# Kernel tuning notes

Measured on AMD Instinct MI355X. Metric: run time of the kernel, lower is better.

Reference implementation:

```python
import jax, jax.numpy as jnp
import numpy as np

N = 16384          # total nodes (128 graphs x 128 ops)
G = 128            # number of graphs
NPG = N // G       # nodes per graph
DIN = 64           # op_input_dim
H = 64             # hidden_dim
BN_EPS = 1e-5


def setup_inputs() -> dict:
    key = jax.random.key(0)
    ks = jax.random.split(key, 16)
    x = jax.random.normal(ks[0], (N, DIN), dtype=jnp.float32)
    # sparse-ish 0/1 adjacency stored dense (as torch.mm path expects); add self-loops so degrees > 0
    u = jax.random.uniform(ks[1], (N, N), dtype=jnp.float32)
    adj = jnp.maximum((u < 0.004).astype(jnp.float32), jnp.eye(N, dtype=jnp.float32))
    # graph_pool: [G, N] average-pooling matrix (block rows of 1/NPG)
    rows = jnp.repeat(jnp.arange(G), NPG)
    graph_pool = jnp.zeros((G, N), jnp.float32).at[rows, jnp.arange(N)].set(1.0 / NPG)
    s = 0.05
    params = {}
    dims_in = [DIN, H]
    for l in range(2):
        d_in = dims_in[l]
        params[f"W1_{l}"] = jax.random.normal(ks[2 + 6 * l], (d_in, H), jnp.float32) * s
        params[f"b1_{l}"] = jnp.zeros((H,), jnp.float32)
        params[f"g1_{l}"] = jnp.ones((H,), jnp.float32)
        params[f"be1_{l}"] = jnp.zeros((H,), jnp.float32)
        params[f"W2_{l}"] = jax.random.normal(ks[3 + 6 * l], (H, H), jnp.float32) * s
        params[f"b2_{l}"] = jnp.zeros((H,), jnp.float32)
        params[f"g_{l}"] = jnp.ones((H,), jnp.float32)   # outer BN gamma
        params[f"be_{l}"] = jnp.zeros((H,), jnp.float32)  # outer BN beta
    return {"x": x, "adj": adj, "graph_pool": graph_pool, **params}


def _bn(h, g, b):
    # training-mode BatchNorm1d over node axis (biased var), eps=1e-5
    m = jnp.mean(h, axis=0)
    v = jnp.var(h, axis=0)
    return g * (h - m) * jax.lax.rsqrt(v + BN_EPS) + b


def _mlp(h, W1, b1, g1, be1, W2, b2):
    # 2-layer MLP: Linear -> BN -> ReLU -> Linear
    return jax.nn.relu(_bn(h @ W1 + b1, g1, be1)) @ W2 + b2


def reference(x, adj, graph_pool,
              W1_0, b1_0, g1_0, be1_0, W2_0, b2_0, g_0, be_0,
              W1_1, b1_1, g1_1, be1_1, W2_1, b2_1, g_1, be_1):
    deg = adj @ jnp.ones((adj.shape[0], 1), adj.dtype)  # [N,1]
    h = x
    layers = [
        (W1_0, b1_0, g1_0, be1_0, W2_0, b2_0, g_0, be_0),
        (W1_1, b1_1, g1_1, be1_1, W2_1, b2_1, g_1, be_1),
    ]
    for (W1, b1, g1, be1, W2, b2, g, be) in layers:
        pooled = (adj @ h) / deg                 # average neighbor aggregation
        pooled_rep = _mlp(pooled, W1, b1, g1, be1, W2, b2)
        h = jax.nn.relu(_bn(pooled_rep, g, be))
    h_nodes = h
    pooled_h = graph_pool @ h                    # [G, H] graph readout
    return (pooled_h, h_nodes)
```

## Files before the change

### kernel.cpp

```cpp
#include <hip/hip_runtime.h>
#include <hip/hip_bf16.h>
#include <stdint.h>

#define N_NODES 16384
#define GG      128
#define HD      64
#define MAXD    192
#define BN_EPS  1e-5f

typedef unsigned short u16;
typedef unsigned int   u32;
typedef unsigned long long u64;

__device__ __forceinline__ float bf2f(u16 u) {
    union { u32 i; float f; } c; c.i = ((u32)u) << 16; return c.f;
}
__device__ __forceinline__ float ldp(const void* p, int i, int flag) {
    return flag ? ((const float*)p)[i] : bf2f(((const u16*)p)[i]);
}

__global__ void k_init(const u32* __restrict__ adj32, double* __restrict__ statsD,
                       int* __restrict__ flag) {
    int i = threadIdx.x;
    if (i < 512) statsD[i] = 0.0;
    if (i == 0) *flag = ((adj32[0] & 0xFFFFu) == 0) ? 1 : 0;
}

__global__ __launch_bounds__(256) void k_agg(
    const void* __restrict__ adjv, const void* __restrict__ xv,
    float* __restrict__ pooled, u16* __restrict__ cols,
    int* __restrict__ cnt, float* __restrict__ invdeg,
    const int* __restrict__ flagp)
{
    const int wave = threadIdx.x >> 6;
    const int lane = threadIdx.x & 63;
    const int row  = blockIdx.x * 4 + wave;
    u16* __restrict__ crow = cols + (size_t)row * MAXD;
    const int flag = *flagp;

    float acc = 0.f;
    int count = 0;

    if (flag) {
        const u32* __restrict__ arow = (const u32*)adjv + (size_t)row * N_NODES;
        const float* __restrict__ x = (const float*)xv;
        uint4 nxt = *(const uint4*)(arow + lane * 4);
        for (int c = 0; c < N_NODES; c += 256) {
            uint4 raw = nxt;
            if (c + 256 < N_NODES)
                nxt = *(const uint4*)(arow + c + 256 + lane * 4);
            const u32 w[4] = {raw.x, raw.y, raw.z, raw.w};
            #pragma unroll
            for (int e = 0; e < 4; ++e) {
                u64 mask = __ballot(w[e] != 0);
                while (mask) {
                    int b = __builtin_ctzll(mask);
                    mask &= mask - 1;
                    int j = c + b * 4 + e;
                    acc += x[(size_t)j * HD + lane];
                    if (lane == 0 && count < MAXD) crow[count] = (u16)j;
                    ++count;
                }
            }
        }
    } else {
        const u16* __restrict__ arow = (const u16*)adjv + (size_t)row * N_NODES;
        const u16* __restrict__ x = (const u16*)xv;
        uint4 nxt = *(const uint4*)(arow + lane * 8);
        for (int c = 0; c < N_NODES; c += 512) {
            uint4 raw = nxt;
            if (c + 512 < N_NODES)
                nxt = *(const uint4*)(arow + c + 512 + lane * 8);
            const u32 w[4] = {raw.x, raw.y, raw.z, raw.w};
            #pragma unroll
            for (int e = 0; e < 8; ++e) {
                u16 u = (u16)(w[e >> 1] >> ((e & 1) * 16));
                u64 mask = __ballot(u != 0);
                while (mask) {
                    int b = __builtin_ctzll(mask);
                    mask &= mask - 1;
                    int j = c + b * 8 + e;
                    acc += bf2f(x[(size_t)j * HD + lane]);
                    if (lane == 0 && count < MAXD) crow[count] = (u16)j;
                    ++count;
                }
            }
        }
    }
    float inv = 1.f / (float)count;
    pooled[(size_t)row * HD + lane] = acc * inv;
    if (lane == 0) { cnt[row] = (count < MAXD) ? count : MAXD; invdeg[row] = inv; }
}

__global__ __launch_bounds__(256) void k_mm(
    const float* __restrict__ src, const void* __restrict__ W,
    const void* __restrict__ bias, float* __restrict__ dst,
    const int* __restrict__ flagp)
{
    __shared__ float Wf[64 * 64];
    __shared__ float S[4 * 64];
    const int tid = threadIdx.x;
    const int flag = *flagp;
    for (int i = tid; i < 64 * 64; i += 256) Wf[i] = ldp(W, i, flag);
    const int rbase = blockIdx.x * 4;
    S[tid] = src[(size_t)rbase * 64 + tid];
    __syncthreads();
    const int f = tid & 63, r = tid >> 6;
    float acc = ldp(bias, f, flag);
    #pragma unroll
    for (int k = 0; k < 64; ++k)
        acc = fmaf(S[r * 64 + k], Wf[k * 64 + f], acc);
    dst[(size_t)(rbase + r) * 64 + f] = acc;
}

__global__ __launch_bounds__(256) void k_stats(
    const float* __restrict__ src, double* __restrict__ statsOut)
{
    __shared__ double shs[256];
    __shared__ double shq[256];
    const int tid = threadIdx.x;
    const int f = tid & 63, rsub = tid >> 6;
    const int rbase = blockIdx.x * 64;
    double s = 0.0, q = 0.0;
    for (int r = rsub; r < 64; r += 4) {
        float v = src[(size_t)(rbase + r) * 64 + f];
        s += (double)v;
        q += (double)v * (double)v;
    }
    shs[tid] = s; shq[tid] = q;
    __syncthreads();
    if (tid < 64) {
        double S = shs[tid] + shs[64 + tid] + shs[128 + tid] + shs[192 + tid];
        double Q = shq[tid] + shq[64 + tid] + shq[128 + tid] + shq[192 + tid];
        atomicAdd(&statsOut[tid], S);
        atomicAdd(&statsOut[64 + tid], Q);
    }
}

__global__ __launch_bounds__(256) void k_bnrelu(
    const float* __restrict__ src, const double* __restrict__ stats,
    const void* __restrict__ g, const void* __restrict__ be,
    float* __restrict__ dst, const int* __restrict__ flagp)
{
    __shared__ float ac[128];
    const int tid = threadIdx.x;
    const int flag = *flagp;
    if (tid < 64) {
        double m = stats[tid] * (1.0 / N_NODES);
        double v = stats[64 + tid] * (1.0 / N_NODES) - m * m;
        float A = ldp(g, tid, flag) / sqrtf((float)v + BN_EPS);
        ac[tid] = A;
        ac[64 + tid] = ldp(be, tid, flag) - (float)m * A;
    }
    __syncthreads();
    const size_t idx = ((size_t)blockIdx.x * 256 + tid) * 4;
    const int f0 = (int)(idx & 63);
    float4 t = *(const float4*)&src[idx];
    const float4 A4 = *(const float4*)&ac[f0];
    const float4 C4 = *(const float4*)&ac[64 + f0];
    float4 r;
    r.x = fmaxf(fmaf(A4.x, t.x, C4.x), 0.f);
    r.y = fmaxf(fmaf(A4.y, t.y, C4.y), 0.f);
    r.z = fmaxf(fmaf(A4.z, t.z, C4.z), 0.f);
    r.w = fmaxf(fmaf(A4.w, t.w, C4.w), 0.f);
    *(float4*)&dst[idx] = r;
}

__global__ __launch_bounds__(256) void k_spmm(
    const float* __restrict__ h, const u16* __restrict__ cols,
    const int* __restrict__ cnt, const float* __restrict__ invdeg,
    float* __restrict__ pooled)
{
    const int wave = threadIdx.x >> 6, lane = threadIdx.x & 63;
    const int row = blockIdx.x * 4 + wave;
    const u16* __restrict__ crow = cols + (size_t)row * MAXD;
    const int n = cnt[row];
    float acc = 0.f;
    for (int k = 0; k < n; ++k)
        acc += h[(size_t)crow[k] * HD + lane];
    pooled[(size_t)row * HD + lane] = acc * invdeg[row];
}

__global__ __launch_bounds__(1024) void k_pool(
    const void* __restrict__ gpv, const float* __restrict__ h,
    float* __restrict__ out, const int* __restrict__ flagp)
{
    __shared__ float red[16 * 64];
    const int g = blockIdx.x;
    const int wave = threadIdx.x >> 6, lane = threadIdx.x & 63;
    const int flag = *flagp;
    float acc = 0.f;
    const int jb0 = wave * (N_NODES / 16);
    if (flag) {
        const float* __restrict__ grow = (const float*)gpv + (size_t)g * N_NODES;
        for (int jb = jb0; jb < jb0 + N_NODES / 16; jb += 4) {
            float4 raw = *(const float4*)(grow + jb);
            if (raw.x != 0.f) acc += raw.x * h[(size_t)(jb + 0) * HD + lane];
            if (raw.y != 0.f) acc += raw.y * h[(size_t)(jb + 1) * HD + lane];
            if (raw.z != 0.f) acc += raw.z * h[(size_t)(jb + 2) * HD + lane];
            if (raw.w != 0.f) acc += raw.w * h[(size_t)(jb + 3) * HD + lane];
        }
    } else {
        const u16* __restrict__ grow = (const u16*)gpv + (size_t)g * N_NODES;
        for (int jb = jb0; jb < jb0 + N_NODES / 16; jb += 8) {
            uint4 raw = *(const uint4*)(grow + jb);
            const u32 w[4] = {raw.x, raw.y, raw.z, raw.w};
            #pragma unroll
            for (int e = 0; e < 8; ++e) {
                u16 u = (u16)(w[e >> 1] >> ((e & 1) * 16));
                if (u) acc += bf2f(u) * h[(size_t)(jb + e) * HD + lane];
            }
        }
    }
    red[wave * 64 + lane] = acc;
    __syncthreads();
    if (wave == 0) {
        float s = 0.f;
        #pragma unroll
        for (int w2 = 0; w2 < 16; ++w2) s += red[w2 * 64 + lane];
        out[g * 64 + lane] = s;
    }
}

extern "C" void kernel_launch(void* const* d_in, const int* in_sizes, int n_in,
                              void* d_out, int out_size, void* d_ws, size_t ws_size,
                              hipStream_t stream)
{
    const void* x    = d_in[0];
    const void* adj  = d_in[1];
    const void* gp   = d_in[2];
    const void* W1_0 = d_in[3];
    const void* b1_0 = d_in[4];
    const void* g1_0 = d_in[5];
    const void* be1_0= d_in[6];
    const void* W2_0 = d_in[7];
    const void* b2_0 = d_in[8];
    const void* g_0  = d_in[9];
    const void* be_0 = d_in[10];
    const void* W1_1 = d_in[11];
    const void* b1_1 = d_in[12];
    const void* g1_1 = d_in[13];
    const void* be1_1= d_in[14];
    const void* W2_1 = d_in[15];
    const void* b2_1 = d_in[16];
    const void* g_1  = d_in[17];
    const void* be_1 = d_in[18];

    char* ws = (char*)d_ws;
    float*  P      = (float*) (ws);
    float*  A      = (float*) (ws + (4u  << 20));
    float*  B      = (float*) (ws + (8u  << 20));
    u16*    cols   = (u16*)   (ws + (12u << 20));
    int*    cnt    = (int*)   (ws + (18u << 20));
    float*  invdeg = (float*) (ws + (18u << 20) + 65536);
    double* sd     = (double*)(ws + (18u << 20) + 131072);
    int*    flag   = (int*)   (ws + (18u << 20) + 131072 + 4096);

    float* out_pool  = (float*)d_out;
    float* out_nodes = (float*)d_out + GG * HD;

    const int EB = (N_NODES * HD / 4) / 256;

    k_init<<<1, 512, 0, stream>>>((const u32*)adj, sd, flag);
    k_agg<<<N_NODES / 4, 256, 0, stream>>>(adj, x, P, cols, cnt, invdeg, flag);

    k_mm<<<N_NODES / 4, 256, 0, stream>>>(P, W1_0, b1_0, A, flag);
    k_stats<<<256, 256, 0, stream>>>(A, sd + 0);
    k_bnrelu<<<EB, 256, 0, stream>>>(A, sd + 0, g1_0, be1_0, B, flag);
    k_mm<<<N_NODES / 4, 256, 0, stream>>>(B, W2_0, b2_0, P, flag);
    k_stats<<<256, 256, 0, stream>>>(P, sd + 128);
    k_bnrelu<<<EB, 256, 0, stream>>>(P, sd + 128, g_0, be_0, A, flag);
    k_spmm<<<N_NODES / 4, 256, 0, stream>>>(A, cols, cnt, invdeg, B);
    k_mm<<<N_NODES / 4, 256, 0, stream>>>(B, W1_1, b1_1, P, flag);
    k_stats<<<256, 256, 0, stream>>>(P, sd + 256);
    k_bnrelu<<<EB, 256, 0, stream>>>(P, sd + 256, g1_1, be1_1, A, flag);
    k_mm<<<N_NODES / 4, 256, 0, stream>>>(A, W2_1, b2_1, B, flag);
    k_stats<<<256, 256, 0, stream>>>(B, sd + 384);
    k_bnrelu<<<EB, 256, 0, stream>>>(B, sd + 384, g_1, be_1, out_nodes, flag);
    k_pool<<<GG, 1024, 0, stream>>>(gp, out_nodes, out_pool, flag);
}
```

Measured before the change: 1.696 ms.

## Split adjacency aggregation into streaming scan with atomics and separate gather

Replaces the per-row wave scan, which interleaved ballot loops with dependent feature gathers, with a grid-stride kernel that streams the dense adjacency and appends nonzero column indices through per-row atomic counters. A separate gather kernel then sums neighbor features from the compacted lists, and the SpMM loops are unrolled by four. The aim is to turn the dominant 1 GiB adjacency read into a pure bandwidth-bound stream. In exchange it adds atomics, a nondeterministic neighbor order (so the float summation order varies), and an extra launch.

After: 1.778 ms. 4.8% more time.

```diff
diff --git a/kernel.cpp b/kernel.cpp
--- a/kernel.cpp
+++ b/kernel.cpp
@@ -19,77 +19,101 @@
     return flag ? ((const float*)p)[i] : bf2f(((const u16*)p)[i]);
 }
 
-__global__ void k_init(const u32* __restrict__ adj32, double* __restrict__ statsD,
-                       int* __restrict__ flag) {
-    int i = threadIdx.x;
-    if (i < 512) statsD[i] = 0.0;
-    if (i == 0) *flag = ((adj32[0] & 0xFFFFu) == 0) ? 1 : 0;
-}
-
-__global__ __launch_bounds__(256) void k_agg(
-    const void* __restrict__ adjv, const void* __restrict__ xv,
-    float* __restrict__ pooled, u16* __restrict__ cols,
-    int* __restrict__ cnt, float* __restrict__ invdeg,
-    const int* __restrict__ flagp)
-{
-    const int wave = threadIdx.x >> 6;
-    const int lane = threadIdx.x & 63;
-    const int row  = blockIdx.x * 4 + wave;
-    u16* __restrict__ crow = cols + (size_t)row * MAXD;
-    const int flag = *flagp;
-
-    float acc = 0.f;
-    int count = 0;
-
+__global__ __launch_bounds__(256) void k_init(
+    const u32* __restrict__ adj32, double* __restrict__ statsD,
+    int* __restrict__ cnt, int* __restrict__ flag)
+{
+    const int gid = blockIdx.x * 256 + threadIdx.x;
+    if (gid < N_NODES) cnt[gid] = 0;
+    if (gid < 512) statsD[gid] = 0.0;
+    if (gid == 0) *flag = ((adj32[0] & 0xFFFFu) == 0) ? 1 : 0;
+}
+
+__global__ __launch_bounds__(256) void k_scan(
+    const void* __restrict__ adjv, u16* __restrict__ cols,
+    int* __restrict__ cnt, const int* __restrict__ flagp)
+{
+    const int flag = *flagp;
+    const size_t stride = (size_t)gridDim.x * 256;
+    size_t i = (size_t)blockIdx.x * 256 + threadIdx.x;
     if (flag) {
-        const u32* __restrict__ arow = (const u32*)adjv + (size_t)row * N_NODES;
-        const float* __restrict__ x = (const float*)xv;
-        uint4 nxt = *(const uint4*)(arow + lane * 4);
-        for (int c = 0; c < N_NODES; c += 256) {
-            uint4 raw = nxt;
-            if (c + 256 < N_NODES)
-                nxt = *(const uint4*)(arow + c + 256 + lane * 4);
-            const u32 w[4] = {raw.x, raw.y, raw.z, raw.w};
-            #pragma unroll
-            for (int e = 0; e < 4; ++e) {
-                u64 mask = __ballot(w[e] != 0);
-                while (mask) {
-                    int b = __builtin_ctzll(mask);
-                    mask &= mask - 1;
-                    int j = c + b * 4 + e;
-                    acc += x[(size_t)j * HD + lane];
-                    if (lane == 0 && count < MAXD) crow[count] = (u16)j;
-                    ++count;
+        const uint4* __restrict__ a = (const uint4*)adjv;
+        const size_t total = (size_t)N_NODES * N_NODES / 4;
+        for (; i < total; i += stride) {
+            uint4 w = a[i];
+            if (w.x | w.y | w.z | w.w) {
+                size_t base = i * 4;
+                int row = (int)(base >> 14);
+                int col = (int)(base & 16383);
+                u16* crow = cols + (size_t)row * MAXD;
+                if (w.x) { int p = atomicAdd(&cnt[row], 1); if (p < MAXD) crow[p] = (u16)(col);     }
+                if (w.y) { int p = atomicAdd(&cnt[row], 1); if (p < MAXD) crow[p] = (u16)(col + 1); }
+                if (w.z) { int p = atomicAdd(&cnt[row], 1); if (p < MAXD) crow[p] = (u16)(col + 2); }
+                if (w.w) { int p = atomicAdd(&cnt[row], 1); if (p < MAXD) crow[p] = (u16)(col + 3); }
+            }
+        }
+    } else {
+        const uint4* __restrict__ a = (const uint4*)adjv;
+        const size_t total = (size_t)N_NODES * N_NODES / 8;
+        for (; i < total; i += stride) {
+            uint4 w = a[i];
+            if (w.x | w.y | w.z | w.w) {
+                size_t base = i * 8;
+                int row = (int)(base >> 14);
+                int col = (int)(base & 16383);
+                u16* crow = cols + (size_t)row * MAXD;
+                const u32 h[4] = {w.x, w.y, w.z, w.w};
+                #pragma unroll
+                for (int e = 0; e < 8; ++e) {
+                    if ((u16)(h[e >> 1] >> ((e & 1) * 16))) {
+                        int p = atomicAdd(&cnt[row], 1);
+                        if (p < MAXD) crow[p] = (u16)(col + e);
+                    }
                 }
             }
         }
+    }
+}
+
+__global__ __launch_bounds__(256) void k_gather(
+    const void* __restrict__ xv, const u16* __restrict__ cols,
+    int* __restrict__ cnt, float* __restrict__ invdeg,
+    float* __restrict__ pooled, const int* __restrict__ flagp)
+{
+    const int wave = threadIdx.x >> 6, lane = threadIdx.x & 63;
+    const int row = blockIdx.x * 4 + wave;
+    const int flag = *flagp;
+    const u16* __restrict__ crow = cols + (size_t)row * MAXD;
+    int n = cnt[row];
+    if (n > MAXD) n = MAXD;
+    float acc = 0.f;
+    int k = 0;
+    if (flag) {
+        const float* __restrict__ x = (const float*)xv;
+        for (; k + 4 <= n; k += 4) {
+            ushort4 j4 = *(const ushort4*)&crow[k];
+            float v0 = x[(size_t)j4.x * HD + lane];
+            float v1 = x[(size_t)j4.y * HD + lane];
+            float v2 = x[(size_t)j4.z * HD + lane];
+            float v3 = x[(size_t)j4.w * HD + lane];
+            acc += (v0 + v1) + (v2 + v3);
+        }
+        for (; k < n; ++k) acc += x[(size_t)crow[k] * HD + lane];
     } else {
-        const u16* __restrict__ arow = (const u16*)adjv + (size_t)row * N_NODES;
         const u16* __restrict__ x = (const u16*)xv;
-        uint4 nxt = *(const uint4*)(arow + lane * 8);
-        for (int c = 0; c < N_NODES; c += 512) {
-            uint4 raw = nxt;
-            if (c + 512 < N_NODES)
-                nxt = *(const uint4*)(arow + c + 512 + lane * 8);
-            const u32 w[4] = {raw.x, raw.y, raw.z, raw.w};
-            #pragma unroll
-            for (int e = 0; e < 8; ++e) {
-                u16 u = (u16)(w[e >> 1] >> ((e & 1) * 16));
-                u64 mask = __ballot(u != 0);
-                while (mask) {
-                    int b = __builtin_ctzll(mask);
-                    mask &= mask - 1;
-                    int j = c + b * 8 + e;
-                    acc += bf2f(x[(size_t)j * HD + lane]);
-                    if (lane == 0 && count < MAXD) crow[count] = (u16)j;
-                    ++count;
-                }
-            }
-        }
-    }
-    float inv = 1.f / (float)count;
+        for (; k + 4 <= n; k += 4) {
+            ushort4 j4 = *(const ushort4*)&crow[k];
+            float v0 = bf2f(x[(size_t)j4.x * HD + lane]);
+            float v1 = bf2f(x[(size_t)j4.y * HD + lane]);
+            float v2 = bf2f(x[(size_t)j4.z * HD + lane]);
+            float v3 = bf2f(x[(size_t)j4.w * HD + lane]);
+            acc += (v0 + v1) + (v2 + v3);
+        }
+        for (; k < n; ++k) acc += bf2f(x[(size_t)crow[k] * HD + lane]);
+    }
+    float inv = 1.f / (float)n;
     pooled[(size_t)row * HD + lane] = acc * inv;
-    if (lane == 0) { cnt[row] = (count < MAXD) ? count : MAXD; invdeg[row] = inv; }
+    if (lane == 0) { invdeg[row] = inv; if (cnt[row] > MAXD) cnt[row] = MAXD; }
 }
 
 __global__ __launch_bounds__(256) void k_mm(
@@ -176,8 +200,16 @@
     const u16* __restrict__ crow = cols + (size_t)row * MAXD;
     const int n = cnt[row];
     float acc = 0.f;
-    for (int k = 0; k < n; ++k)
-        acc += h[(size_t)crow[k] * HD + lane];
+    int k = 0;
+    for (; k + 4 <= n; k += 4) {
+        ushort4 j4 = *(const ushort4*)&crow[k];
+        float v0 = h[(size_t)j4.x * HD + lane];
+        float v1 = h[(size_t)j4.y * HD + lane];
+        float v2 = h[(size_t)j4.z * HD + lane];
+        float v3 = h[(size_t)j4.w * HD + lane];
+        acc += (v0 + v1) + (v2 + v3);
+    }
+    for (; k < n; ++k) acc += h[(size_t)crow[k] * HD + lane];
     pooled[(size_t)row * HD + lane] = acc * invdeg[row];
 }
 
@@ -261,8 +293,9 @@
 
     const int EB = (N_NODES * HD / 4) / 256;
 
-    k_init<<<1, 512, 0, stream>>>((const u32*)adj, sd, flag);
-    k_agg<<<N_NODES / 4, 256, 0, stream>>>(adj, x, P, cols, cnt, invdeg, flag);
+    k_init<<<N_NODES / 256, 256, 0, stream>>>((const u32*)adj, sd, cnt, flag);
+    k_scan<<<16384, 256, 0, stream>>>(adj, cols, cnt, flag);
+    k_gather<<<N_NODES / 4, 256, 0, stream>>>(x, cols, cnt, invdeg, P, flag);
 
     k_mm<<<N_NODES / 4, 256, 0, stream>>>(P, W1_0, b1_0, A, flag);
     k_stats<<<256, 256, 0, stream>>>(A, sd + 0);
```
